# Kernel tuning notes

Measured on AMD Instinct MI355X. Metric: run time of the kernel, lower is better.

## Reference

```python
import jax, jax.numpy as jnp
import numpy as np
from jax.scipy.ndimage import map_coordinates

# module hyperparameters (match init_kwargs)
N = 64          # patch size
GRIDSIZE = 2
C = GRIDSIZE * GRIDSIZE   # channels = patches per solution region
PADDED = 192    # padded canvas size
B = 512


def setup_inputs() -> dict:
    key = jax.random.key(0)
    k1, k2 = jax.random.split(key)
    patches = jax.random.normal(k1, (B, N, N, C), dtype=jnp.float32)
    # sub-pixel scan offsets (dx, dy); keep translated patch inside the canvas
    max_off = (PADDED - N) / 2.0 - 1.0
    positions = jax.random.uniform(k2, (B, 1, 2, C), dtype=jnp.float32,
                                   minval=-max_off, maxval=max_off)
    return {"patches": patches, "positions": positions}


def _translate_one(img, txy):
    # img: (P, P); txy = (dx, dy). tfa.image.translate semantics:
    # out(y, x) = img(y - dy, x - dx), bilinear interpolation, zero fill.
    P = img.shape[0]
    grid = jnp.arange(P, dtype=img.dtype)
    rows = jnp.broadcast_to(grid[:, None] - txy[1], (P, P))
    cols = jnp.broadcast_to(grid[None, :] - txy[0], (P, P))
    return map_coordinates(img, [rows, cols], order=1, mode='constant', cval=0.0)


def reference(patches, positions):
    Bv, Nv, _, Cv = patches.shape
    pad_lo = (PADDED - Nv) // 2
    pad_hi = PADDED - Nv - pad_lo
    # center-pad each NxN patch into the padded canvas
    padded = jnp.pad(patches, ((0, 0), (pad_lo, pad_hi), (pad_lo, pad_hi), (0, 0)))
    # channel -> flat: (B*C, P, P)
    imgs = padded.transpose(0, 3, 1, 2).reshape(Bv * Cv, PADDED, PADDED)
    # (B,1,2,C) -> (B*C, 2) as (dx, dy)
    offs = positions[:, 0].transpose(0, 2, 1).reshape(Bv * Cv, 2)
    translated = jax.vmap(_translate_one)(imgs, offs)
    # sum translated patches over the channel axis -> (B, P, P, 1)
    out = translated.reshape(Bv, Cv, PADDED, PADDED).sum(axis=1)[..., None]
    return out
```

## Files before the change

### kernel.cpp

```cpp
#include <hip/hip_runtime.h>

#define PATCH_N 64
#define CH      4
#define PADDED  192
#define BATCH   512
#define THREADS 1024
#define RSTRIDE 76
#define PLANE_F (PATCH_N * RSTRIDE)
#define LDS_F   (CH * PLANE_F)

__device__ __forceinline__ int   rfl_i(int x)   { return __builtin_amdgcn_readfirstlane(x); }
__device__ __forceinline__ float rfl_f(float x) { return __int_as_float(__builtin_amdgcn_readfirstlane(__float_as_int(x))); }

__global__ __launch_bounds__(THREADS, 8)
void reassemble_v7(const float* __restrict__ patches,
                   const float* __restrict__ positions,
                   float* __restrict__ out)
{
    __shared__ float4 lds4[LDS_F / 4];
    float* __restrict__ lds = reinterpret_cast<float*>(lds4);

    const int b   = blockIdx.x;
    const int tid = threadIdx.x;

    const float* pos = positions + (size_t)b * 8;
    int   syc[CH], sxc[CH], pc[CH], Qc[CH];
    float wx0c[CH], wx1c[CH], wy0c[CH], wy1c[CH];
#pragma unroll
    for (int c = 0; c < CH; ++c) {
        const float tx  = 64.f + rfl_f(pos[c]);
        const float sxf = ceilf(tx);
        sxc[c]  = rfl_i((int)sxf);
        wx1c[c] = rfl_f(sxf - tx);
        wx0c[c] = 1.f - wx1c[c];
        const float ty  = 64.f + rfl_f(pos[CH + c]);
        const float syf = ceilf(ty);
        syc[c]  = rfl_i((int)syf);
        wy1c[c] = rfl_f(syf - ty);
        wy0c[c] = 1.f - wy1c[c];
        pc[c] = sxc[c] & 3;
        Qc[c] = 4 - (sxc[c] & ~3);
    }

    {
        const int row = tid / 12;
        const int m   = tid - row * 12;
#pragma unroll
        for (int c = 0; c < CH; ++c) {
            if (tid < 768) {
                const int col = (m <= pc[c] + 3) ? m : (m + 64);
                lds[c * PLANE_F + row * RSTRIDE + col] = 0.f;
            }
        }
    }
    __syncthreads();

    const float4* __restrict__ p4 =
        reinterpret_cast<const float4*>(patches) + (size_t)b * (PATCH_N * PATCH_N);
#pragma unroll
    for (int i = 0; i < (PATCH_N * PATCH_N) / THREADS; ++i) {
        const int pix = i * THREADS + tid;
        const int r   = pix >> 6;
        const int xcl = pix & 63;
        const float4 v = p4[pix];
        lds[0 * PLANE_F + r * RSTRIDE + xcl + pc[0] + 4] = v.x;
        lds[1 * PLANE_F + r * RSTRIDE + xcl + pc[1] + 4] = v.y;
        lds[2 * PLANE_F + r * RSTRIDE + xcl + pc[2] + 4] = v.z;
        lds[3 * PLANE_F + r * RSTRIDE + xcl + pc[3] + 4] = v.w;
    }
    __syncthreads();

    float4* __restrict__ o4 =
        reinterpret_cast<float4*>(out) + (size_t)b * (PADDED * PADDED / 4);

#pragma unroll
    for (int it = 0; it < (PADDED * PADDED / 4) / THREADS; ++it) {
        const int idx = it * THREADS + tid;
        const int y   = idx / 48;
        const int x0  = (idx - y * 48) << 2;
        float a0 = 0.f, a1 = 0.f, a2 = 0.f, a3 = 0.f;

#pragma unroll
        for (int c = 0; c < CH; ++c) {
            const int r0 = y - syc[c];
            const int j0 = x0 - sxc[c];
            const bool act = ((unsigned)(r0 + 1) <= 64u) && ((unsigned)(j0 + 4) <= 67u);
            if (__ballot(act) == 0ull) continue;

            const int q   = min(max(x0 + Qc[c], 0), 68);
            const int r0c = min(max(r0, 0), 63);
            const int r1c = min(max(r0 + 1, 0), 63);
            const int A0  = c * PLANE_F + r0c * RSTRIDE + q;
            const int A1  = c * PLANE_F + r1c * RSTRIDE + q;
            const float4 W0  = lds4[A0 >> 2];
            const float  W04 = lds[A0 + 4];
            const float4 W1  = lds4[A1 >> 2];
            const float  W14 = lds[A1 + 4];

            const float wy0m = ((unsigned)r0       < 64u) ? wy0c[c] : 0.f;
            const float wy1m = ((unsigned)(r0 + 1) < 64u) ? wy1c[c] : 0.f;

            const bool v0 = (unsigned)(j0    ) < 64u;
            const bool v1 = (unsigned)(j0 + 1) < 64u;
            const bool v2 = (unsigned)(j0 + 2) < 64u;
            const bool v3 = (unsigned)(j0 + 3) < 64u;
            const bool v4 = (unsigned)(j0 + 4) < 64u;
            const float wx0 = wx0c[c], wx1 = wx1c[c];
            const float l0 = v0 ? wx0 : 0.f, rw0 = v1 ? wx1 : 0.f;
            const float l1 = v1 ? wx0 : 0.f, rw1 = v2 ? wx1 : 0.f;
            const float l2 = v2 ? wx0 : 0.f, rw2 = v3 ? wx1 : 0.f;
            const float l3 = v3 ? wx0 : 0.f, rw3 = v4 ? wx1 : 0.f;

            float t0, t1;
            t0 = fmaf(rw0, W0.y, l0 * W0.x);  t1 = fmaf(rw0, W1.y, l0 * W1.x);
            a0 = fmaf(wy0m, t0, fmaf(wy1m, t1, a0));
            t0 = fmaf(rw1, W0.z, l1 * W0.y);  t1 = fmaf(rw1, W1.z, l1 * W1.y);
            a1 = fmaf(wy0m, t0, fmaf(wy1m, t1, a1));
            t0 = fmaf(rw2, W0.w, l2 * W0.z);  t1 = fmaf(rw2, W1.w, l2 * W1.z);
            a2 = fmaf(wy0m, t0, fmaf(wy1m, t1, a2));
            t0 = fmaf(rw3, W04,  l3 * W0.w);  t1 = fmaf(rw3, W14,  l3 * W1.w);
            a3 = fmaf(wy0m, t0, fmaf(wy1m, t1, a3));
        }

        o4[idx] = make_float4(a0, a1, a2, a3);
    }
}

extern "C" void kernel_launch(void* const* d_in, const int* in_sizes, int n_in,
                              void* d_out, int out_size, void* d_ws, size_t ws_size,
                              hipStream_t stream) {
    const float* patches   = (const float*)d_in[0];
    const float* positions = (const float*)d_in[1];
    float* out = (float*)d_out;

    reassemble_v7<<<dim3(BATCH), THREADS, 0, stream>>>(patches, positions, out);
}
```

Measured before the change: 102.5 us.

## Precompute horizontal interpolation into zero-padded LDS planes, simplify output pass

Bilinear interpolation is split into two passes. The horizontal pass happens while loading patches: each thread combines a pixel with its right neighbour through a wave shuffle and stores the result into zero-bordered LDS planes that now carry two extra rows. The output loop then does only a vertical blend of two aligned float4 reads per channel, dropping the per-pixel mask logic and the scalar extra loads. In exchange the whole LDS area is zeroed, the channel-skip test becomes a coarser wave-uniform row check, and the load phase does more work.

```diff
diff --git a/kernel.cpp b/kernel.cpp
--- a/kernel.cpp
+++ b/kernel.cpp
@@ -5,32 +5,35 @@
 #define PADDED  192
 #define BATCH   512
 #define THREADS 1024
-#define RSTRIDE 76
-#define PLANE_F (PATCH_N * RSTRIDE)
+#define PROWS   66
+#define PCOLS   76
+#define PLANE_F (PROWS * PCOLS)
 #define LDS_F   (CH * PLANE_F)
 
 __device__ __forceinline__ int   rfl_i(int x)   { return __builtin_amdgcn_readfirstlane(x); }
 __device__ __forceinline__ float rfl_f(float x) { return __int_as_float(__builtin_amdgcn_readfirstlane(__float_as_int(x))); }
 
 __global__ __launch_bounds__(THREADS, 8)
-void reassemble_v7(const float* __restrict__ patches,
-                   const float* __restrict__ positions,
-                   float* __restrict__ out)
+void reassemble_h(const float* __restrict__ patches,
+                  const float* __restrict__ positions,
+                  float* __restrict__ out)
 {
     __shared__ float4 lds4[LDS_F / 4];
     float* __restrict__ lds = reinterpret_cast<float*>(lds4);
 
-    const int b   = blockIdx.x;
-    const int tid = threadIdx.x;
+    const int b    = blockIdx.x;
+    const int tid  = threadIdx.x;
+    const int lane = tid & 63;
+    const int wid  = rfl_i(tid >> 6);
 
     const float* pos = positions + (size_t)b * 8;
-    int   syc[CH], sxc[CH], pc[CH], Qc[CH];
+    int   syc[CH], ac[CH], padc[CH];
     float wx0c[CH], wx1c[CH], wy0c[CH], wy1c[CH];
 #pragma unroll
     for (int c = 0; c < CH; ++c) {
         const float tx  = 64.f + rfl_f(pos[c]);
         const float sxf = ceilf(tx);
-        sxc[c]  = rfl_i((int)sxf);
+        const int   sx  = rfl_i((int)sxf);
         wx1c[c] = rfl_f(sxf - tx);
         wx0c[c] = 1.f - wx1c[c];
         const float ty  = 64.f + rfl_f(pos[CH + c]);
@@ -38,35 +41,34 @@
         syc[c]  = rfl_i((int)syf);
         wy1c[c] = rfl_f(syf - ty);
         wy0c[c] = 1.f - wy1c[c];
-        pc[c] = sxc[c] & 3;
-        Qc[c] = 4 - (sxc[c] & ~3);
+        ac[c]   = (sx - 1) >> 2;
+        padc[c] = (sx - 1) & 3;
     }
 
-    {
-        const int row = tid / 12;
-        const int m   = tid - row * 12;
 #pragma unroll
-        for (int c = 0; c < CH; ++c) {
-            if (tid < 768) {
-                const int col = (m <= pc[c] + 3) ? m : (m + 64);
-                lds[c * PLANE_F + row * RSTRIDE + col] = 0.f;
-            }
-        }
+    for (int j = 0; j < (LDS_F / 4 + THREADS - 1) / THREADS; ++j) {
+        const int idx = j * THREADS + tid;
+        if (idx < LDS_F / 4) lds4[idx] = make_float4(0.f, 0.f, 0.f, 0.f);
     }
     __syncthreads();
 
     const float4* __restrict__ p4 =
         reinterpret_cast<const float4*>(patches) + (size_t)b * (PATCH_N * PATCH_N);
+    const bool last = (lane == 63);
 #pragma unroll
-    for (int i = 0; i < (PATCH_N * PATCH_N) / THREADS; ++i) {
-        const int pix = i * THREADS + tid;
-        const int r   = pix >> 6;
-        const int xcl = pix & 63;
-        const float4 v = p4[pix];
-        lds[0 * PLANE_F + r * RSTRIDE + xcl + pc[0] + 4] = v.x;
-        lds[1 * PLANE_F + r * RSTRIDE + xcl + pc[1] + 4] = v.y;
-        lds[2 * PLANE_F + r * RSTRIDE + xcl + pc[2] + 4] = v.z;
-        lds[3 * PLANE_F + r * RSTRIDE + xcl + pc[3] + 4] = v.w;
+    for (int pass = 0; pass < 4; ++pass) {
+        const int r = pass * 16 + wid;
+        const float4 v = p4[r * PATCH_N + lane];
+#pragma unroll
+        for (int c = 0; c < CH; ++c) {
+            const float val = (c == 0) ? v.x : (c == 1) ? v.y : (c == 2) ? v.z : v.w;
+            float vr = __shfl_down(val, 1);
+            vr = last ? 0.f : vr;
+            const float h = fmaf(wx1c[c], vr, wx0c[c] * val);
+            float* pl = lds + c * PLANE_F + (r + 1) * PCOLS;
+            pl[lane + padc[c] + 5] = h;
+            if (lane == 0) pl[padc[c] + 4] = wx1c[c] * val;
+        }
     }
     __syncthreads();
 
@@ -77,49 +79,28 @@
     for (int it = 0; it < (PADDED * PADDED / 4) / THREADS; ++it) {
         const int idx = it * THREADS + tid;
         const int y   = idx / 48;
-        const int x0  = (idx - y * 48) << 2;
+        const int xg  = idx - y * 48;
+        const int y0  = rfl_i(y);
+        const int yp1 = y + 1;
         float a0 = 0.f, a1 = 0.f, a2 = 0.f, a3 = 0.f;
 
 #pragma unroll
         for (int c = 0; c < CH; ++c) {
-            const int r0 = y - syc[c];
-            const int j0 = x0 - sxc[c];
-            const bool act = ((unsigned)(r0 + 1) <= 64u) && ((unsigned)(j0 + 4) <= 67u);
-            if (__ballot(act) == 0ull) continue;
+            if (y0 + 2 < syc[c] - 1 || y0 > syc[c] + 63) continue;
 
-            const int q   = min(max(x0 + Qc[c], 0), 68);
-            const int r0c = min(max(r0, 0), 63);
-            const int r1c = min(max(r0 + 1, 0), 63);
-            const int A0  = c * PLANE_F + r0c * RSTRIDE + q;
-            const int A1  = c * PLANE_F + r1c * RSTRIDE + q;
-            const float4 W0  = lds4[A0 >> 2];
-            const float  W04 = lds[A0 + 4];
-            const float4 W1  = lds4[A1 >> 2];
-            const float  W14 = lds[A1 + 4];
+            const int t    = yp1 - syc[c];
+            const int row0 = min(max(t, 0), 65);
+            const int row1 = min(max(t, -1), 64) + 1;
+            const int q4   = min(max(xg - ac[c] + 1, 0), 18);
+            const int base = c * (PLANE_F / 4) + q4;
+            const float4 W0 = lds4[base + row0 * (PCOLS / 4)];
+            const float4 W1 = lds4[base + row1 * (PCOLS / 4)];
 
-            const float wy0m = ((unsigned)r0       < 64u) ? wy0c[c] : 0.f;
-            const float wy1m = ((unsigned)(r0 + 1) < 64u) ? wy1c[c] : 0.f;
-
-            const bool v0 = (unsigned)(j0    ) < 64u;
-            const bool v1 = (unsigned)(j0 + 1) < 64u;
-            const bool v2 = (unsigned)(j0 + 2) < 64u;
-            const bool v3 = (unsigned)(j0 + 3) < 64u;
-            const bool v4 = (unsigned)(j0 + 4) < 64u;
-            const float wx0 = wx0c[c], wx1 = wx1c[c];
-            const float l0 = v0 ? wx0 : 0.f, rw0 = v1 ? wx1 : 0.f;
-            const float l1 = v1 ? wx0 : 0.f, rw1 = v2 ? wx1 : 0.f;
-            const float l2 = v2 ? wx0 : 0.f, rw2 = v3 ? wx1 : 0.f;
-            const float l3 = v3 ? wx0 : 0.f, rw3 = v4 ? wx1 : 0.f;
-
-            float t0, t1;
-            t0 = fmaf(rw0, W0.y, l0 * W0.x);  t1 = fmaf(rw0, W1.y, l0 * W1.x);
-            a0 = fmaf(wy0m, t0, fmaf(wy1m, t1, a0));
-            t0 = fmaf(rw1, W0.z, l1 * W0.y);  t1 = fmaf(rw1, W1.z, l1 * W1.y);
-            a1 = fmaf(wy0m, t0, fmaf(wy1m, t1, a1));
-            t0 = fmaf(rw2, W0.w, l2 * W0.z);  t1 = fmaf(rw2, W1.w, l2 * W1.z);
-            a2 = fmaf(wy0m, t0, fmaf(wy1m, t1, a2));
-            t0 = fmaf(rw3, W04,  l3 * W0.w);  t1 = fmaf(rw3, W14,  l3 * W1.w);
-            a3 = fmaf(wy0m, t0, fmaf(wy1m, t1, a3));
+            const float wy0 = wy0c[c], wy1 = wy1c[c];
+            a0 = fmaf(wy0, W0.x, a0); a0 = fmaf(wy1, W1.x, a0);
+            a1 = fmaf(wy0, W0.y, a1); a1 = fmaf(wy1, W1.y, a1);
+            a2 = fmaf(wy0, W0.z, a2); a2 = fmaf(wy1, W1.z, a2);
+            a3 = fmaf(wy0, W0.w, a3); a3 = fmaf(wy1, W1.w, a3);
         }
 
         o4[idx] = make_float4(a0, a1, a2, a3);
@@ -133,5 +114,5 @@
     const float* positions = (const float*)d_in[1];
     float* out = (float*)d_out;
 
-    reassemble_v7<<<dim3(BATCH), THREADS, 0, stream>>>(patches, positions, out);
+    reassemble_h<<<dim3(BATCH), THREADS, 0, stream>>>(patches, positions, out);
 }
```

After: 98.25 us. 1.04x faster.
